# Kernel optimization log

Hardware: AMD Instinct MI355X
Metric: run time of the kernel (lower is better)

## Reference

```python
import jax, jax.numpy as jnp
from jax import lax
import numpy as np

NUM_EMBEDDINGS = 512
EMBEDDING_DIM = 64
COMMITMENT_COST = 0.25
SPARSITY_LEVEL = 8


def batch_omp(data, dictionary, max_nonzero):
    """Batch-OMP (Rubinstein et al.).
    data: [D, N], dictionary: [D, K] (columns unit-norm). Returns gamma [K, N].
    Runs a fixed max_nonzero greedy steps (the torch tolerance 1e-7 never
    triggers early exit on random data).
    """
    D, N = data.shape
    K = dictionary.shape[1]
    G = dictionary.T @ dictionary                 # [K, K] Gram matrix
    h_bar = (dictionary.T @ data).T               # [N, K] initial correlations
    h = h_bar
    mask = jnp.zeros((N, K), dtype=bool)          # selected-atom indicator
    rows = jnp.arange(N)
    L = jnp.ones((N, 1, 1), dtype=data.dtype)     # incremental Cholesky of G[I,I]
    I = None                                      # [N, k] selected indices
    x = jnp.zeros((N, K), dtype=data.dtype)
    for k in range(1, max_nonzero + 1):
        # greedy atom selection (masking already-chosen atoms)
        idx = jnp.argmax(jnp.abs(h * (~mask).astype(h.dtype)), axis=1)   # [N]
        mask = mask.at[rows, idx].set(True)
        if k > 1:
            g = G[I, idx[:, None]][..., None]                            # [N, k-1, 1]
            w = lax.linalg.triangular_solve(L, g, left_side=True, lower=True)
            w = jnp.swapaxes(w, 1, 2)                                    # [N, 1, k-1]
            w_corner = jnp.sqrt(1.0 - jnp.sum(w * w, axis=2, keepdims=True))
            top = jnp.concatenate([L, jnp.zeros((N, k - 1, 1), L.dtype)], axis=2)
            bot = jnp.concatenate([w, w_corner], axis=2)
            L = jnp.concatenate([top, bot], axis=1)                      # [N, k, k]
            I = jnp.concatenate([I, idx[:, None]], axis=1)
        else:
            I = idx[:, None]
        hb = jnp.take_along_axis(h_bar, I, axis=1)[..., None]            # [N, k, 1]
        # cholesky_solve: L L^T x = hb
        y = lax.linalg.triangular_solve(L, hb, left_side=True, lower=True)
        xs = lax.linalg.triangular_solve(L, y, left_side=True, lower=True,
                                         transpose_a=True)              # [N, k, 1]
        x = jnp.zeros((N, K), data.dtype).at[rows[:, None], I].set(xs[..., 0])
        beta = x @ G                                                     # x is zero off-support
        h = h_bar - beta
    return x.T                                                           # [K, N]


def setup_inputs() -> dict:
    key = jax.random.key(0)
    k1, k2 = jax.random.split(key)
    z_e = jax.random.normal(k1, (32, EMBEDDING_DIM, 32, 32), dtype=jnp.float32)
    dictionary = jax.random.normal(k2, (EMBEDDING_DIM, NUM_EMBEDDINGS), dtype=jnp.float32)
    beta = jnp.array([1.0 - COMMITMENT_COST], dtype=jnp.float32)  # nn.Parameter(1 - commitment_cost)
    return {"z_e": z_e, "dictionary": dictionary, "beta": beta}


def reference(z_e, dictionary, beta):
    # straight-through column normalization (torch does it via .data assignment)
    Dn_val = dictionary / jnp.linalg.norm(dictionary, axis=0)
    Dn = dictionary + lax.stop_gradient(Dn_val - dictionary)
    zp = jnp.transpose(z_e, (0, 2, 3, 1))                 # [B, H, W, C]
    ze_shape = zp.shape
    zf = zp.reshape(EMBEDDING_DIM, -1)                    # view(D, -1): [D, N]
    gamma = lax.stop_gradient(batch_omp(zf, Dn, SPARSITY_LEVEL))   # [K, N]; copied via .data in torch
    recon = Dn @ gamma                                    # [D, N]
    e_latent_loss = jnp.mean((lax.stop_gradient(recon) - zf) ** 2)
    q_loss = jnp.mean((recon - lax.stop_gradient(zf)) ** 2)
    loss = e_latent_loss * COMMITMENT_COST + beta[0] * q_loss
    recon_st = zf + lax.stop_gradient(recon - zf)         # straight-through
    sm = jax.nn.softmax(gamma, axis=0)
    perplexity = jnp.exp(-jnp.mean(jnp.sum(sm * jnp.log(sm + 1e-10), axis=0)))
    recon_out = jnp.transpose(recon_st.reshape(ze_shape), (0, 3, 1, 2))
    return loss, recon_out, lax.stop_gradient(zf), perplexity, gamma
```

## Files before the change

kernel.cpp:

```cpp
#include <hip/hip_runtime.h>
#include <math.h>

#define NCOL 32768
#define KAT  512
#define DIM  64

#define O_LOSS  0
#define O_RECON 1
#define O_ZF    2097153
#define O_PERP  4194305
#define O_GAMMA 4194306

#define WS_DN   0
#define WS_DNT  32768
#define WS_G    65536
#define WS_ACC  327680

__device__ __forceinline__ float wave_max_bcast_f32(float v) {
    int x = __float_as_int(v);
    int t;
    t = __builtin_amdgcn_update_dpp(x, x, 0x111, 0xf, 0xf, false);
    x = __float_as_int(fmaxf(__int_as_float(x), __int_as_float(t)));
    t = __builtin_amdgcn_update_dpp(x, x, 0x112, 0xf, 0xf, false);
    x = __float_as_int(fmaxf(__int_as_float(x), __int_as_float(t)));
    t = __builtin_amdgcn_update_dpp(x, x, 0x114, 0xf, 0xf, false);
    x = __float_as_int(fmaxf(__int_as_float(x), __int_as_float(t)));
    t = __builtin_amdgcn_update_dpp(x, x, 0x118, 0xf, 0xf, false);
    x = __float_as_int(fmaxf(__int_as_float(x), __int_as_float(t)));
    t = __builtin_amdgcn_update_dpp(x, x, 0x142, 0xa, 0xf, false);
    x = __float_as_int(fmaxf(__int_as_float(x), __int_as_float(t)));
    t = __builtin_amdgcn_update_dpp(x, x, 0x143, 0xc, 0xf, false);
    x = __float_as_int(fmaxf(__int_as_float(x), __int_as_float(t)));
    return __int_as_float(__builtin_amdgcn_readlane(x, 63));
}

__device__ __forceinline__ unsigned wave_min_bcast_u32(unsigned v) {
    int x = (int)v;
    int t;
    t = __builtin_amdgcn_update_dpp(x, x, 0x111, 0xf, 0xf, false);
    x = (int)min((unsigned)x, (unsigned)t);
    t = __builtin_amdgcn_update_dpp(x, x, 0x112, 0xf, 0xf, false);
    x = (int)min((unsigned)x, (unsigned)t);
    t = __builtin_amdgcn_update_dpp(x, x, 0x114, 0xf, 0xf, false);
    x = (int)min((unsigned)x, (unsigned)t);
    t = __builtin_amdgcn_update_dpp(x, x, 0x118, 0xf, 0xf, false);
    x = (int)min((unsigned)x, (unsigned)t);
    t = __builtin_amdgcn_update_dpp(x, x, 0x142, 0xa, 0xf, false);
    x = (int)min((unsigned)x, (unsigned)t);
    t = __builtin_amdgcn_update_dpp(x, x, 0x143, 0xc, 0xf, false);
    x = (int)min((unsigned)x, (unsigned)t);
    return (unsigned)__builtin_amdgcn_readlane(x, 63);
}

__global__ void prep_kernel(const float* __restrict__ dict, float* __restrict__ ws) {
    float* Dn  = ws + WS_DN;
    float* DnT = ws + WS_DNT;
    float* acc = ws + WS_ACC;
    int a = threadIdx.x;
    if (a < 2) acc[a] = 0.f;
    float s = 0.f;
    #pragma unroll
    for (int d = 0; d < DIM; ++d) { float v = dict[d*KAT + a]; s += v * v; }
    float nrm = sqrtf(s);
    #pragma unroll
    for (int d = 0; d < DIM; ++d) {
        float v = dict[d*KAT + a] / nrm;
        Dn[d*KAT + a]  = v;
        DnT[a*DIM + d] = v;
    }
}

__global__ void gram_kernel(const float* __restrict__ ws_in, float* __restrict__ ws) {
    const float* Dn = ws_in + WS_DN;
    float* G = ws + WS_G;
    int i = blockIdx.x, j = threadIdx.x;
    float s = 0.f;
    #pragma unroll
    for (int d = 0; d < DIM; ++d)
        s = fmaf(Dn[d*KAT + i], Dn[d*KAT + j], s);
    G[i*KAT + j] = s;
}

__global__ __launch_bounds__(256) void zf_kernel(const float* __restrict__ z_e,
                                                 float* __restrict__ out) {
    __shared__ float tile[64 * 33];
    int s = blockIdx.x;
    int b = s >> 5, h = s & 31;
    int t = threadIdx.x;
    int srcbase = b * 65536 + h * 32;
    #pragma unroll
    for (int i = 0; i < 8; ++i) {
        int e = t + i * 256;
        int c = e >> 5, w = e & 31;
        tile[c * 33 + w] = z_e[srcbase + c * 1024 + w];
    }
    __syncthreads();
    int obase = O_ZF + s * 2048;
    #pragma unroll
    for (int i = 0; i < 8; ++i) {
        int e = t + i * 256;
        out[obase + e] = tile[(e & 63) * 33 + (e >> 6)];
    }
}

__global__ void gzero_kernel(float2* __restrict__ g2) {
    int id = blockIdx.x * 256 + threadIdx.x;
    #pragma unroll
    for (int i = 0; i < 4; ++i)
        g2[id + i * 2097152] = make_float2(0.f, 0.f);
}

__global__ __launch_bounds__(256) void omp_kernel(const float* __restrict__ z_e,
                                                  const float* __restrict__ ws,
                                                  float* __restrict__ out,
                                                  float* __restrict__ wsw) {
    const float* Dn  = ws + WS_DN;
    const float* DnT = ws + WS_DNT;
    const float* G   = ws + WS_G;
    float* acc = wsw + WS_ACC;

    __shared__ float xcols[DIM * 16];
    __shared__ float hbar[16 * KAT];

    const int t = threadIdx.x;
    const int n_base = blockIdx.x * 16;

    #pragma unroll
    for (int i = 0; i < 4; ++i) {
        int e = t + i * 256;
        int d = e >> 4, c = e & 15;
        int L = d * NCOL + n_base + c;
        int src = (L >> 16) * 65536 + (L & 63) * 1024 + (((L >> 11) & 31) << 5) + ((L >> 6) & 31);
        xcols[e] = z_e[src];
    }
    __syncthreads();

    {
        float a0[16], a1[16];
        #pragma unroll
        for (int i = 0; i < 16; ++i) { a0[i] = 0.f; a1[i] = 0.f; }
        const float4* xc4 = (const float4*)xcols;
        for (int d = 0; d < DIM; ++d) {
            float v0 = Dn[d * KAT + t];
            float v1 = Dn[d * KAT + 256 + t];
            #pragma unroll
            for (int q = 0; q < 4; ++q) {
                float4 xv = xc4[d * 4 + q];
                a0[q*4+0] = fmaf(v0, xv.x, a0[q*4+0]);
                a0[q*4+1] = fmaf(v0, xv.y, a0[q*4+1]);
                a0[q*4+2] = fmaf(v0, xv.z, a0[q*4+2]);
                a0[q*4+3] = fmaf(v0, xv.w, a0[q*4+3]);
                a1[q*4+0] = fmaf(v1, xv.x, a1[q*4+0]);
                a1[q*4+1] = fmaf(v1, xv.y, a1[q*4+1]);
                a1[q*4+2] = fmaf(v1, xv.z, a1[q*4+2]);
                a1[q*4+3] = fmaf(v1, xv.w, a1[q*4+3]);
            }
        }
        #pragma unroll
        for (int c = 0; c < 16; ++c) {
            hbar[c * KAT + t]       = a0[c];
            hbar[c * KAT + 256 + t] = a1[c];
        }
    }
    __syncthreads();

    const int wv = t >> 6, lane = t & 63;
    float wv_sq = 0.f, wv_S = 0.f;

    #pragma unroll 1
    for (int cc = 0; cc < 4; ++cc) {
        const int col = wv * 4 + cc;
        const int n = n_base + col;
        const float* hbcol = hbar + col * KAT;

        float h[8];
        #pragma unroll
        for (int r = 0; r < 8; ++r) h[r] = hbcol[(r << 6) + lane];

        unsigned msk = 0;
        float uv[56];
        float Lr[28];
        float invd[8], yv[8], xr[8];
        int Iv[8];

        #pragma unroll
        for (int k = 0; k < 8; ++k) {
            float bv = -1.f; int bi = 0; float hb = 0.f;
            #pragma unroll
            for (int r = 0; r < 8; ++r) {
                float av = ((msk >> r) & 1) ? -1.f : fabsf(h[r]);
                bool gt = av > bv;
                bv = gt ? av : bv;
                bi = gt ? ((r << 6) | lane) : bi;
                hb = gt ? h[r] : hb;
            }
            float maxv = wave_max_bcast_f32(bv);
            unsigned cand = (bv == maxv) ? (unsigned)bi : 0xffffffffu;
            const int idx = (int)wave_min_bcast_u32(cand);
            unsigned long long sm = __ballot((bv == maxv) && (bi == idx) && (hb < 0.f));
            float hwin = (sm != 0ull) ? -maxv : maxv;

            if ((idx & 63) == lane) msk |= 1u << (idx >> 6);
            Iv[k] = idx;

            const float* grow = G + idx * KAT;
            float gk[8];
            if (k < 7) {
                #pragma unroll
                for (int r = 0; r < 8; ++r) gk[r] = grow[(r << 6) + lane];
            }

            float Lk[7];
            if (k == 0) {
                invd[0] = 1.f;
            } else {
                float s2 = 0.f;
                #pragma unroll
                for (int i = 0; i < 7; ++i) if (i < k) {
                    float a = grow[Iv[i]];
                    #pragma unroll
                    for (int j = 0; j < 7; ++j) if (j < i) a = fmaf(-Lr[i*(i-1)/2 + j], Lk[j], a);
                    Lk[i] = a * invd[i];
                    s2 = fmaf(Lk[i], Lk[i], s2);
                }
                #pragma unroll
                for (int j = 0; j < 7; ++j) if (j < k) Lr[k*(k-1)/2 + j] = Lk[j];
                invd[k] = 1.f / sqrtf(1.f - s2);
            }
            yv[k] = hwin * invd[k];

            if (k < 7) {
                #pragma unroll
                for (int r = 0; r < 8; ++r) {
                    float a = gk[r];
                    #pragma unroll
                    for (int j = 0; j < 7; ++j) if (j < k) a = fmaf(-Lk[j], uv[j*8 + r], a);
                    a *= invd[k];
                    uv[k*8 + r] = a;
                    h[r] = fmaf(-yv[k], a, h[r]);
                }
            }
        }

        #pragma unroll
        for (int i = 7; i >= 0; --i) {
            float a = yv[i];
            #pragma unroll
            for (int j = 0; j < 8; ++j) if (j > i) a = fmaf(-Lr[j*(j-1)/2 + i], xr[j], a);
            xr[i] = a * invd[i];
        }

        #pragma unroll
        for (int j = 0; j < 8; ++j)
            if (lane == j) out[O_GAMMA + Iv[j] * NCOL + n] = xr[j];

        float rec = 0.f;
        #pragma unroll
        for (int j = 0; j < 8; ++j)
            rec = fmaf(xr[j], DnT[Iv[j] * DIM + lane], rec);
        int L = lane * NCOL + n;
        int perm = (L >> 16) * 65536 + (L & 63) * 1024 + (((L >> 11) & 31) << 5) + ((L >> 6) & 31);
        out[O_RECON + perm] = rec;

        float xd = xcols[lane * 16 + col];
        float diff = rec - xd;
        float sq = diff * diff;
        #pragma unroll
        for (int off = 32; off; off >>= 1) sq += __shfl_xor(sq, off, 64);
        if (lane == 0) wv_sq += sq;

        {
            float m = 0.f;
            #pragma unroll
            for (int j = 0; j < 8; ++j) m = fmaxf(m, xr[j]);
            float xsel = 0.f;
            #pragma unroll
            for (int j = 0; j < 8; ++j) xsel = (lane == j) ? xr[j] : xsel;
            float e = (lane < 8) ? expf(xsel - m) : 0.f;
            float se = e;
            #pragma unroll
            for (int off = 1; off < 8; off <<= 1) se += __shfl_xor(se, off, 64);
            float e0 = expf(-m);
            float Z = fmaf(504.f, e0, se);
            float invZ = 1.f / Z;
            float p = e * invZ;
            float tq = (lane < 8) ? p * logf(p + 1e-10f) : 0.f;
            #pragma unroll
            for (int off = 1; off < 8; off <<= 1) tq += __shfl_xor(tq, off, 64);
            if (lane == 0) {
                float p0 = e0 * invZ;
                wv_S += tq + 504.f * p0 * logf(p0 + 1e-10f);
            }
        }
    }

    if (lane == 0) {
        atomicAdd(&acc[0], wv_sq);
        atomicAdd(&acc[1], wv_S);
    }
}

__global__ void fin_kernel(const float* __restrict__ ws, const float* __restrict__ beta,
                           float* __restrict__ out) {
    const float* acc = ws + WS_ACC;
    float mse = acc[0] / 2097152.f;
    out[O_LOSS] = mse * 0.25f + beta[0] * mse;
    out[O_PERP] = expf(-acc[1] / 32768.f);
}

extern "C" void kernel_launch(void* const* d_in, const int* in_sizes, int n_in,
                              void* d_out, int out_size, void* d_ws, size_t ws_size,
                              hipStream_t stream) {
    const float* z_e  = (const float*)d_in[0];
    const float* dict = (const float*)d_in[1];
    const float* beta = (const float*)d_in[2];
    float* out = (float*)d_out;
    float* ws  = (float*)d_ws;

    prep_kernel<<<1, 512, 0, stream>>>(dict, ws);
    gram_kernel<<<512, 512, 0, stream>>>(ws, ws);
    zf_kernel<<<1024, 256, 0, stream>>>(z_e, out);
    gzero_kernel<<<8192, 256, 0, stream>>>((float2*)(out + O_GAMMA));
    omp_kernel<<<2048, 256, 0, stream>>>(z_e, ws, out, ws);
    fin_kernel<<<1, 1, 0, stream>>>(ws, beta, out);
}
```

Baseline: 372.3 us.

## Fuse launches and interleave two OMP columns per wave for ILP

Merges dictionary normalization into the gamma-zeroing kernel, writes zf from inside the OMP kernel's column load (dropping the separate transpose kernel), and finalizes loss and perplexity through a last-block atomic counter instead of a separate kernel. The OMP loop now processes two columns per wave at once, so the independent reductions and Cholesky updates can overlap, and launch bounds request two blocks per SM. The cost is much higher register pressure from doubled per-column state, which may spill, and block 0 of the init kernel does all the normalization work serially.

Measured after the change: 542.1 us. 1.46x slower.

```diff
diff --git a/kernel.cpp b/kernel.cpp
--- a/kernel.cpp
+++ b/kernel.cpp
@@ -52,21 +52,35 @@
     return (unsigned)__builtin_amdgcn_readlane(x, 63);
 }
 
-__global__ void prep_kernel(const float* __restrict__ dict, float* __restrict__ ws) {
-    float* Dn  = ws + WS_DN;
-    float* DnT = ws + WS_DNT;
-    float* acc = ws + WS_ACC;
-    int a = threadIdx.x;
-    if (a < 2) acc[a] = 0.f;
-    float s = 0.f;
+__global__ __launch_bounds__(256) void init_kernel(const float* __restrict__ dict,
+                                                   float* __restrict__ ws,
+                                                   float* __restrict__ out) {
+    int id = blockIdx.x * 256 + threadIdx.x;
+    float2* g2 = (float2*)(out + O_GAMMA);
     #pragma unroll
-    for (int d = 0; d < DIM; ++d) { float v = dict[d*KAT + a]; s += v * v; }
-    float nrm = sqrtf(s);
-    #pragma unroll
-    for (int d = 0; d < DIM; ++d) {
-        float v = dict[d*KAT + a] / nrm;
-        Dn[d*KAT + a]  = v;
-        DnT[a*DIM + d] = v;
+    for (int i = 0; i < 4; ++i)
+        g2[id + i * 2097152] = make_float2(0.f, 0.f);
+
+    if (blockIdx.x == 0) {
+        float* Dn  = ws + WS_DN;
+        float* DnT = ws + WS_DNT;
+        float* acc = ws + WS_ACC;
+        int t = threadIdx.x;
+        if (t == 0) { acc[0] = 0.f; acc[1] = 0.f; ((unsigned*)acc)[2] = 0u; }
+        #pragma unroll
+        for (int half = 0; half < 2; ++half) {
+            int a = t + half * 256;
+            float s = 0.f;
+            #pragma unroll
+            for (int d = 0; d < DIM; ++d) { float v = dict[d*KAT + a]; s += v * v; }
+            float nrm = sqrtf(s);
+            #pragma unroll
+            for (int d = 0; d < DIM; ++d) {
+                float v = dict[d*KAT + a] / nrm;
+                Dn[d*KAT + a]  = v;
+                DnT[a*DIM + d] = v;
+            }
+        }
     }
 }
 
@@ -81,39 +95,11 @@
     G[i*KAT + j] = s;
 }
 
-__global__ __launch_bounds__(256) void zf_kernel(const float* __restrict__ z_e,
-                                                 float* __restrict__ out) {
-    __shared__ float tile[64 * 33];
-    int s = blockIdx.x;
-    int b = s >> 5, h = s & 31;
-    int t = threadIdx.x;
-    int srcbase = b * 65536 + h * 32;
-    #pragma unroll
-    for (int i = 0; i < 8; ++i) {
-        int e = t + i * 256;
-        int c = e >> 5, w = e & 31;
-        tile[c * 33 + w] = z_e[srcbase + c * 1024 + w];
-    }
-    __syncthreads();
-    int obase = O_ZF + s * 2048;
-    #pragma unroll
-    for (int i = 0; i < 8; ++i) {
-        int e = t + i * 256;
-        out[obase + e] = tile[(e & 63) * 33 + (e >> 6)];
-    }
-}
-
-__global__ void gzero_kernel(float2* __restrict__ g2) {
-    int id = blockIdx.x * 256 + threadIdx.x;
-    #pragma unroll
-    for (int i = 0; i < 4; ++i)
-        g2[id + i * 2097152] = make_float2(0.f, 0.f);
-}
-
-__global__ __launch_bounds__(256) void omp_kernel(const float* __restrict__ z_e,
-                                                  const float* __restrict__ ws,
-                                                  float* __restrict__ out,
-                                                  float* __restrict__ wsw) {
+__global__ __launch_bounds__(256, 2) void omp_kernel(const float* __restrict__ z_e,
+                                                     const float* __restrict__ ws,
+                                                     float* __restrict__ out,
+                                                     const float* __restrict__ beta,
+                                                     float* __restrict__ wsw) {
     const float* Dn  = ws + WS_DN;
     const float* DnT = ws + WS_DNT;
     const float* G   = ws + WS_G;
@@ -129,9 +115,11 @@
     for (int i = 0; i < 4; ++i) {
         int e = t + i * 256;
         int d = e >> 4, c = e & 15;
-        int L = d * NCOL + n_base + c;
-        int src = (L >> 16) * 65536 + (L & 63) * 1024 + (((L >> 11) & 31) << 5) + ((L >> 6) & 31);
-        xcols[e] = z_e[src];
+        int Lf = d * NCOL + n_base + c;
+        int src = (Lf >> 16) * 65536 + (Lf & 63) * 1024 + (((Lf >> 11) & 31) << 5) + ((Lf >> 6) & 31);
+        float v = z_e[src];
+        xcols[e] = v;
+        out[O_ZF + Lf] = v;
     }
     __syncthreads();
 
@@ -168,128 +156,150 @@
     float wv_sq = 0.f, wv_S = 0.f;
 
     #pragma unroll 1
-    for (int cc = 0; cc < 4; ++cc) {
-        const int col = wv * 4 + cc;
-        const int n = n_base + col;
-        const float* hbcol = hbar + col * KAT;
-
-        float h[8];
-        #pragma unroll
-        for (int r = 0; r < 8; ++r) h[r] = hbcol[(r << 6) + lane];
-
-        unsigned msk = 0;
-        float uv[56];
-        float Lr[28];
-        float invd[8], yv[8], xr[8];
-        int Iv[8];
+    for (int pp = 0; pp < 2; ++pp) {
+        const int col0 = wv * 4 + pp * 2;
+
+        float h[2][8];
+        unsigned msk[2] = {0u, 0u};
+        float uv[2][56], Lr[2][28], invd[2][8], yv[2][8], xr[2][8];
+        int Iv[2][8];
+
+        #pragma unroll
+        for (int q = 0; q < 2; ++q)
+            #pragma unroll
+            for (int r = 0; r < 8; ++r)
+                h[q][r] = hbar[(col0 + q) * KAT + (r << 6) + lane];
 
         #pragma unroll
         for (int k = 0; k < 8; ++k) {
-            float bv = -1.f; int bi = 0; float hb = 0.f;
-            #pragma unroll
-            for (int r = 0; r < 8; ++r) {
-                float av = ((msk >> r) & 1) ? -1.f : fabsf(h[r]);
-                bool gt = av > bv;
-                bv = gt ? av : bv;
-                bi = gt ? ((r << 6) | lane) : bi;
-                hb = gt ? h[r] : hb;
-            }
-            float maxv = wave_max_bcast_f32(bv);
-            unsigned cand = (bv == maxv) ? (unsigned)bi : 0xffffffffu;
-            const int idx = (int)wave_min_bcast_u32(cand);
-            unsigned long long sm = __ballot((bv == maxv) && (bi == idx) && (hb < 0.f));
-            float hwin = (sm != 0ull) ? -maxv : maxv;
-
-            if ((idx & 63) == lane) msk |= 1u << (idx >> 6);
-            Iv[k] = idx;
-
-            const float* grow = G + idx * KAT;
-            float gk[8];
-            if (k < 7) {
-                #pragma unroll
-                for (int r = 0; r < 8; ++r) gk[r] = grow[(r << 6) + lane];
-            }
-
-            float Lk[7];
-            if (k == 0) {
-                invd[0] = 1.f;
-            } else {
-                float s2 = 0.f;
-                #pragma unroll
-                for (int i = 0; i < 7; ++i) if (i < k) {
-                    float a = grow[Iv[i]];
+            float bv[2]; int bi[2]; float hb[2];
+            #pragma unroll
+            for (int q = 0; q < 2; ++q) {
+                bv[q] = -1.f; bi[q] = 0; hb[q] = 0.f;
+                #pragma unroll
+                for (int r = 0; r < 8; ++r) {
+                    float av = ((msk[q] >> r) & 1) ? -1.f : fabsf(h[q][r]);
+                    bool gt = av > bv[q];
+                    bv[q] = gt ? av : bv[q];
+                    bi[q] = gt ? ((r << 6) | lane) : bi[q];
+                    hb[q] = gt ? h[q][r] : hb[q];
+                }
+            }
+            float maxv[2];
+            maxv[0] = wave_max_bcast_f32(bv[0]);
+            maxv[1] = wave_max_bcast_f32(bv[1]);
+            unsigned cand0 = (bv[0] == maxv[0]) ? (unsigned)bi[0] : 0xffffffffu;
+            unsigned cand1 = (bv[1] == maxv[1]) ? (unsigned)bi[1] : 0xffffffffu;
+            int idx[2];
+            idx[0] = (int)wave_min_bcast_u32(cand0);
+            idx[1] = (int)wave_min_bcast_u32(cand1);
+
+            float hwin[2], gk[2][8];
+            const float* grow[2];
+            #pragma unroll
+            for (int q = 0; q < 2; ++q) {
+                unsigned long long sm =
+                    __ballot((bv[q] == maxv[q]) && (bi[q] == idx[q]) && (hb[q] < 0.f));
+                hwin[q] = (sm != 0ull) ? -maxv[q] : maxv[q];
+                if ((idx[q] & 63) == lane) msk[q] |= 1u << (idx[q] >> 6);
+                Iv[q][k] = idx[q];
+                grow[q] = G + idx[q] * KAT;
+                if (k < 7) {
                     #pragma unroll
-                    for (int j = 0; j < 7; ++j) if (j < i) a = fmaf(-Lr[i*(i-1)/2 + j], Lk[j], a);
-                    Lk[i] = a * invd[i];
-                    s2 = fmaf(Lk[i], Lk[i], s2);
-                }
-                #pragma unroll
-                for (int j = 0; j < 7; ++j) if (j < k) Lr[k*(k-1)/2 + j] = Lk[j];
-                invd[k] = 1.f / sqrtf(1.f - s2);
-            }
-            yv[k] = hwin * invd[k];
-
-            if (k < 7) {
-                #pragma unroll
-                for (int r = 0; r < 8; ++r) {
-                    float a = gk[r];
+                    for (int r = 0; r < 8; ++r) gk[q][r] = grow[q][(r << 6) + lane];
+                }
+            }
+
+            #pragma unroll
+            for (int q = 0; q < 2; ++q) {
+                float Lk[7];
+                if (k == 0) {
+                    invd[q][0] = 1.f;
+                } else {
+                    float s2 = 0.f;
                     #pragma unroll
-                    for (int j = 0; j < 7; ++j) if (j < k) a = fmaf(-Lk[j], uv[j*8 + r], a);
-                    a *= invd[k];
-                    uv[k*8 + r] = a;
-                    h[r] = fmaf(-yv[k], a, h[r]);
-                }
-            }
-        }
-
-        #pragma unroll
-        for (int i = 7; i >= 0; --i) {
-            float a = yv[i];
-            #pragma unroll
-            for (int j = 0; j < 8; ++j) if (j > i) a = fmaf(-Lr[j*(j-1)/2 + i], xr[j], a);
-            xr[i] = a * invd[i];
-        }
-
-        #pragma unroll
-        for (int j = 0; j < 8; ++j)
-            if (lane == j) out[O_GAMMA + Iv[j] * NCOL + n] = xr[j];
-
-        float rec = 0.f;
-        #pragma unroll
-        for (int j = 0; j < 8; ++j)
-            rec = fmaf(xr[j], DnT[Iv[j] * DIM + lane], rec);
-        int L = lane * NCOL + n;
-        int perm = (L >> 16) * 65536 + (L & 63) * 1024 + (((L >> 11) & 31) << 5) + ((L >> 6) & 31);
-        out[O_RECON + perm] = rec;
-
-        float xd = xcols[lane * 16 + col];
-        float diff = rec - xd;
-        float sq = diff * diff;
-        #pragma unroll
-        for (int off = 32; off; off >>= 1) sq += __shfl_xor(sq, off, 64);
-        if (lane == 0) wv_sq += sq;
-
-        {
-            float m = 0.f;
-            #pragma unroll
-            for (int j = 0; j < 8; ++j) m = fmaxf(m, xr[j]);
-            float xsel = 0.f;
-            #pragma unroll
-            for (int j = 0; j < 8; ++j) xsel = (lane == j) ? xr[j] : xsel;
-            float e = (lane < 8) ? expf(xsel - m) : 0.f;
-            float se = e;
-            #pragma unroll
-            for (int off = 1; off < 8; off <<= 1) se += __shfl_xor(se, off, 64);
-            float e0 = expf(-m);
-            float Z = fmaf(504.f, e0, se);
-            float invZ = 1.f / Z;
-            float p = e * invZ;
-            float tq = (lane < 8) ? p * logf(p + 1e-10f) : 0.f;
-            #pragma unroll
-            for (int off = 1; off < 8; off <<= 1) tq += __shfl_xor(tq, off, 64);
-            if (lane == 0) {
-                float p0 = e0 * invZ;
-                wv_S += tq + 504.f * p0 * logf(p0 + 1e-10f);
+                    for (int i = 0; i < 7; ++i) if (i < k) {
+                        float a = grow[q][Iv[q][i]];
+                        #pragma unroll
+                        for (int j = 0; j < 7; ++j) if (j < i)
+                            a = fmaf(-Lr[q][i*(i-1)/2 + j], Lk[j], a);
+                        Lk[i] = a * invd[q][i];
+                        s2 = fmaf(Lk[i], Lk[i], s2);
+                    }
+                    #pragma unroll
+                    for (int j = 0; j < 7; ++j) if (j < k) Lr[q][k*(k-1)/2 + j] = Lk[j];
+                    invd[q][k] = 1.f / sqrtf(1.f - s2);
+                }
+                yv[q][k] = hwin[q] * invd[q][k];
+
+                if (k < 7) {
+                    #pragma unroll
+                    for (int r = 0; r < 8; ++r) {
+                        float a = gk[q][r];
+                        #pragma unroll
+                        for (int j = 0; j < 7; ++j) if (j < k)
+                            a = fmaf(-Lk[j], uv[q][j*8 + r], a);
+                        a *= invd[q][k];
+                        uv[q][k*8 + r] = a;
+                        h[q][r] = fmaf(-yv[q][k], a, h[q][r]);
+                    }
+                }
+            }
+        }
+
+        #pragma unroll
+        for (int q = 0; q < 2; ++q) {
+            #pragma unroll
+            for (int i = 7; i >= 0; --i) {
+                float a = yv[q][i];
+                #pragma unroll
+                for (int j = 0; j < 8; ++j) if (j > i)
+                    a = fmaf(-Lr[q][j*(j-1)/2 + i], xr[q][j], a);
+                xr[q][i] = a * invd[q][i];
+            }
+            const int n = n_base + col0 + q;
+
+            #pragma unroll
+            for (int j = 0; j < 8; ++j)
+                if (lane == j) out[O_GAMMA + Iv[q][j] * NCOL + n] = xr[q][j];
+
+            float rec = 0.f;
+            #pragma unroll
+            for (int j = 0; j < 8; ++j)
+                rec = fmaf(xr[q][j], DnT[Iv[q][j] * DIM + lane], rec);
+            int Lf = lane * NCOL + n;
+            int perm = (Lf >> 16) * 65536 + (Lf & 63) * 1024 + (((Lf >> 11) & 31) << 5) + ((Lf >> 6) & 31);
+            out[O_RECON + perm] = rec;
+
+            float xd = xcols[lane * 16 + col0 + q];
+            float diff = rec - xd;
+            float sq = diff * diff;
+            #pragma unroll
+            for (int off = 32; off; off >>= 1) sq += __shfl_xor(sq, off, 64);
+            if (lane == 0) wv_sq += sq;
+
+            {
+                float m = 0.f;
+                #pragma unroll
+                for (int j = 0; j < 8; ++j) m = fmaxf(m, xr[q][j]);
+                float xsel = 0.f;
+                #pragma unroll
+                for (int j = 0; j < 8; ++j) xsel = (lane == j) ? xr[q][j] : xsel;
+                float e = (lane < 8) ? expf(xsel - m) : 0.f;
+                float se = e;
+                #pragma unroll
+                for (int off = 1; off < 8; off <<= 1) se += __shfl_xor(se, off, 64);
+                float e0 = expf(-m);
+                float Z = fmaf(504.f, e0, se);
+                float invZ = 1.f / Z;
+                float p = e * invZ;
+                float tq = (lane < 8) ? p * logf(p + 1e-10f) : 0.f;
+                #pragma unroll
+                for (int off = 1; off < 8; off <<= 1) tq += __shfl_xor(tq, off, 64);
+                if (lane == 0) {
+                    float p0 = e0 * invZ;
+                    wv_S += tq + 504.f * p0 * logf(p0 + 1e-10f);
+                }
             }
         }
     }
@@ -298,14 +308,19 @@
         atomicAdd(&acc[0], wv_sq);
         atomicAdd(&acc[1], wv_S);
     }
-}
-
-__global__ void fin_kernel(const float* __restrict__ ws, const float* __restrict__ beta,
-                           float* __restrict__ out) {
-    const float* acc = ws + WS_ACC;
-    float mse = acc[0] / 2097152.f;
-    out[O_LOSS] = mse * 0.25f + beta[0] * mse;
-    out[O_PERP] = expf(-acc[1] / 32768.f);
+    __threadfence();
+    __syncthreads();
+    if (t == 0) {
+        unsigned old = atomicAdd((unsigned*)acc + 2, 1u);
+        if (old == gridDim.x - 1) {
+            __threadfence();
+            float s0 = atomicAdd(&acc[0], 0.f);
+            float s1 = atomicAdd(&acc[1], 0.f);
+            float mse = s0 / 2097152.f;
+            out[O_LOSS] = mse * 0.25f + beta[0] * mse;
+            out[O_PERP] = expf(-s1 / 32768.f);
+        }
+    }
 }
 
 extern "C" void kernel_launch(void* const* d_in, const int* in_sizes, int n_in,
@@ -317,10 +332,7 @@
     float* out = (float*)d_out;
     float* ws  = (float*)d_ws;
 
-    prep_kernel<<<1, 512, 0, stream>>>(dict, ws);
+    init_kernel<<<8192, 256, 0, stream>>>(dict, ws, out);
     gram_kernel<<<512, 512, 0, stream>>>(ws, ws);
-    zf_kernel<<<1024, 256, 0, stream>>>(z_e, out);
-    gzero_kernel<<<8192, 256, 0, stream>>>((float2*)(out + O_GAMMA));
-    omp_kernel<<<2048, 256, 0, stream>>>(z_e, ws, out, ws);
-    fin_kernel<<<1, 1, 0, stream>>>(ws, beta, out);
-}
+    omp_kernel<<<2048, 256, 0, stream>>>(z_e, ws, out, beta, ws);
+}
```
